# Optimization experiments

Measured on AMD Instinct MI355X. Metric: run time of the kernel, lower is better.

## Reference

```python
import jax, jax.numpy as jnp
import numpy as np

B, H, N, D = 16, 2048, 1024, 2048  # batch, seq len, vocab_size, d_model (= 2*vocab)
KAPPA = 1.0
SCALE = 0.02  # std for materialized params (original inits to zeros -> trivial output)


def setup_inputs() -> dict:
    key = jax.random.key(0)
    kz, kf, kv, kw = jax.random.split(key, 4)
    z = jax.random.randint(kz, (B, H), 0, N)
    F_mat = jax.random.normal(kf, (D, D), jnp.float32) * SCALE
    V = jax.random.normal(kv, (D, D), jnp.float32) * SCALE
    W = jax.random.normal(kw, (D, D), jnp.float32) * SCALE
    return {"z": z, "F_mat": F_mat, "V": V, "W": W}


def reference(z, F_mat, V, W):
    # x[b,t] = e_{z[b,t]} + e_{N + z[b,t-1]},  x[b,0] = e_{z[b,0]}  (E / E_tilde basis rows)
    z_prev = jnp.roll(z, 1, axis=1).at[:, 0].set(0)
    E_z = jax.nn.one_hot(z, D, dtype=jnp.float32)          # [B,H,D]
    x = E_z + jax.nn.one_hot(z_prev + N, D, dtype=jnp.float32)
    x = x.at[:, 0, :].set(E_z[:, 0, :])

    x_H = x[:, -1, :]                                      # [B,D] single query
    W_x = jnp.einsum('bhd,ed->bhe', x, W)                  # x @ W.T -> [B,H,D]
    scores = jnp.einsum('bd,bhd->bh', x_H, W_x)            # [B,H]
    attn = jax.nn.softmax(scores, axis=-1)                 # att_type='softmax'
    weighted_sum = jnp.einsum('bh,bhd->bd', attn, x)       # [B,D]

    # U.T @ (.) just takes the first N coordinates (U = E.T, identity columns)
    xi_A = (weighted_sum @ V.T)[:, :N]                     # [B,N]
    combined = x_H + KAPPA * weighted_sum
    xi_F = (combined @ F_mat.T)[:, :N]                     # [B,N]
    xi = xi_A + xi_F
    # match torch output shape [B, N, 1]
    return xi[..., None], xi_A[..., None], xi_F[..., None]
```

## Files before the change

### kernel.cpp

```cpp
#include <hip/hip_runtime.h>

#define BB 16
#define HH 2048
#define NN 1024
#define DD 2048


__global__ __launch_bounds__(1024) void ot_phase1(const int* __restrict__ z,
                                                  const float* __restrict__ W,
                                                  int* __restrict__ hdr,
                                                  float* __restrict__ wsT) {
    __shared__ int   zsh[HH];
    __shared__ float w1s[DD];
    __shared__ float w2s[DD];
    __shared__ float ws[DD];
    __shared__ float red[16];

    const int b    = blockIdx.x;
    const int tid  = threadIdx.x;
    const int lane = tid & 63;
    const int wid  = tid >> 6;

    ((int2*)zsh)[tid] = ((const int2*)(z + (size_t)b * HH))[tid];
    ws[tid] = 0.f;
    ws[tid + 1024] = 0.f;
    __syncthreads();

    const int d1 = zsh[HH - 1];
    const int d2 = zsh[HH - 2] + NN;

    if (tid < 512) ((float4*)w1s)[tid]       = ((const float4*)(W + (size_t)d1 * DD))[tid];
    else           ((float4*)w2s)[tid - 512] = ((const float4*)(W + (size_t)d2 * DD))[tid - 512];
    __syncthreads();

    const int h0 = tid * 2, h1 = h0 + 1;
    const int z0 = zsh[h0], z1 = zsh[h1];
    const int p0 = (h0 > 0) ? zsh[h0 - 1] + NN : 0;
    const int p1 = z0 + NN;

    float s0 = w1s[z0] + w2s[z0];
    if (h0 > 0) s0 += w1s[p0] + w2s[p0];
    float s1 = w1s[z1] + w2s[z1] + w1s[p1] + w2s[p1];

    float m = fmaxf(s0, s1);
#pragma unroll
    for (int off = 32; off > 0; off >>= 1) m = fmaxf(m, __shfl_xor(m, off));
    if (lane == 0) red[wid] = m;
    __syncthreads();
    float mx = red[0];
#pragma unroll
    for (int i = 1; i < 16; ++i) mx = fmaxf(mx, red[i]);

    const float e0 = __expf(s0 - mx);
    const float e1 = __expf(s1 - mx);
    float t = e0 + e1;
#pragma unroll
    for (int off = 32; off > 0; off >>= 1) t += __shfl_xor(t, off);
    __syncthreads();
    if (lane == 0) red[wid] = t;
    __syncthreads();
    float tot = red[0];
#pragma unroll
    for (int i = 1; i < 16; ++i) tot += red[i];
    const float inv = 1.f / tot;

    atomicAdd(&ws[z0], e0);
    if (h0 > 0) atomicAdd(&ws[p0], e0);
    atomicAdd(&ws[z1], e1);
    atomicAdd(&ws[p1], e1);
    __syncthreads();

    if (tid < 512) {
        float4 o;
        o.x = ws[4 * tid + 0] * inv;
        o.y = ws[4 * tid + 1] * inv;
        o.z = ws[4 * tid + 2] * inv;
        o.w = ws[4 * tid + 3] * inv;
        ((float4*)wsT)[(size_t)tid * BB + b] = o;
    }
    if (tid == 0) { hdr[b] = d1; hdr[BB + b] = d2; }
}

__global__ __launch_bounds__(512) void ot_phase2(const float* __restrict__ V,
                                                 const float* __restrict__ F,
                                                 const int* __restrict__ hdr,
                                                 const float* __restrict__ wsT,
                                                 float* __restrict__ out) {
    const int tid  = threadIdx.x;
    const int lane = tid & 63;
    const int w    = tid >> 6;
    const int bq   = lane & 15;
    const int q    = lane >> 4;
    const int slot = w * 4 + q;
    const int n0   = blockIdx.x;
    const int n1   = n0 + 512;

    const float4* __restrict__ V0 = (const float4*)(V + (size_t)n0 * DD);
    const float4* __restrict__ F0 = (const float4*)(F + (size_t)n0 * DD);
    const float4* __restrict__ V1 = (const float4*)(V + (size_t)n1 * DD);
    const float4* __restrict__ F1 = (const float4*)(F + (size_t)n1 * DD);
    const float4* __restrict__ WS = (const float4*)wsT;

    float a0 = 0.f, f0 = 0.f, a1 = 0.f, f1 = 0.f;

#pragma unroll 4
    for (int it = 0; it < 16; ++it) {
        const int dg = it * 32 + slot;
        float4 s  = WS[(size_t)dg * BB + bq];
        float4 v0 = V0[dg];
        float4 g0 = F0[dg];
        float4 v1 = V1[dg];
        float4 g1 = F1[dg];
        a0 += v0.x * s.x + v0.y * s.y + v0.z * s.z + v0.w * s.w;
        f0 += g0.x * s.x + g0.y * s.y + g0.z * s.z + g0.w * s.w;
        a1 += v1.x * s.x + v1.y * s.y + v1.z * s.z + v1.w * s.w;
        f1 += g1.x * s.x + g1.y * s.y + g1.z * s.z + g1.w * s.w;
    }

#pragma unroll
    for (int off = 16; off <= 32; off <<= 1) {
        a0 += __shfl_xor(a0, off);
        f0 += __shfl_xor(f0, off);
        a1 += __shfl_xor(a1, off);
        f1 += __shfl_xor(f1, off);
    }

    __shared__ float red[4][8][BB];
    if (lane < 16) {
        red[0][w][bq] = a0;
        red[1][w][bq] = f0;
        red[2][w][bq] = a1;
        red[3][w][bq] = f1;
    }
    __syncthreads();

    if (tid < BB) {
        const int b = tid;
        float A0 = 0.f, Fv0 = 0.f, A1 = 0.f, Fv1 = 0.f;
#pragma unroll
        for (int ww = 0; ww < 8; ++ww) {
            A0  += red[0][ww][b];
            Fv0 += red[1][ww][b];
            A1  += red[2][ww][b];
            Fv1 += red[3][ww][b];
        }
        const int e1i = hdr[b], e2i = hdr[BB + b];
        const float* __restrict__ Fr0 = F + (size_t)n0 * DD;
        const float* __restrict__ Fr1 = F + (size_t)n1 * DD;
        Fv0 += Fr0[e1i] + Fr0[e2i];
        Fv1 += Fr1[e1i] + Fr1[e2i];
        out[(size_t)b * NN + n0]            = A0 + Fv0;
        out[(size_t)(BB + b) * NN + n0]     = A0;
        out[(size_t)(2 * BB + b) * NN + n0] = Fv0;
        out[(size_t)b * NN + n1]            = A1 + Fv1;
        out[(size_t)(BB + b) * NN + n1]     = A1;
        out[(size_t)(2 * BB + b) * NN + n1] = Fv1;
    }
}

extern "C" void kernel_launch(void* const* d_in, const int* in_sizes, int n_in,
                              void* d_out, int out_size, void* d_ws, size_t ws_size,
                              hipStream_t stream) {
    const int*   z     = (const int*)d_in[0];
    const float* F_mat = (const float*)d_in[1];
    const float* V     = (const float*)d_in[2];
    const float* W     = (const float*)d_in[3];
    float* out = (float*)d_out;

    int*   hdr = (int*)d_ws;
    float* wsT = (float*)((char*)d_ws + 128);

    ot_phase1<<<BB, 1024, 0, stream>>>(z, W, hdr, wsT);
    ot_phase2<<<NN / 2, 512, 0, stream>>>(V, F_mat, hdr, wsT, out);
}
```

Measured before the change: 25.77 us.

## Pack attention sums to bf16, process four output rows per block, prefetch W row

Phase 1 now reads the last two tokens directly and issues the W row loads before the z tile is staged, which removes one barrier. It also stores the normalized weighted sums as packed bf16. Phase 2 preloads each thread's weighted-sum slice into registers once and processes four V/F rows per block instead of two, so each slice is reused across eight dot products and the wsT traffic is halved. The bf16 packing adds rounding error to the weighted sums, and the larger per-thread register set may limit occupancy.

```diff
diff --git a/kernel.cpp b/kernel.cpp
--- a/kernel.cpp
+++ b/kernel.cpp
@@ -4,36 +4,45 @@
 #define HH 2048
 #define NN 1024
 #define DD 2048
+#define DG (DD / 4)
 
+
+__device__ __forceinline__ unsigned short f2bf(float f) {
+    unsigned u = __float_as_uint(f);
+    u += 0x7fffu + ((u >> 16) & 1u);
+    return (unsigned short)(u >> 16);
+}
 
 __global__ __launch_bounds__(1024) void ot_phase1(const int* __restrict__ z,
                                                   const float* __restrict__ W,
                                                   int* __restrict__ hdr,
-                                                  float* __restrict__ wsT) {
+                                                  uint2* __restrict__ wsB) {
     __shared__ int   zsh[HH];
     __shared__ float w1s[DD];
     __shared__ float w2s[DD];
-    __shared__ float ws[DD];
-    __shared__ float red[16];
+    __shared__ float wsh[DD];
+    __shared__ float redm[16], redt[16];
 
     const int b    = blockIdx.x;
     const int tid  = threadIdx.x;
     const int lane = tid & 63;
     const int wid  = tid >> 6;
 
+    const int4 zt = ((const int4*)(z + (size_t)b * HH))[DG - 1];
+    const int d1 = zt.w;
+    const int d2 = zt.z + NN;
+
+    float4 wv;
+    if (tid < 512) wv = ((const float4*)(W + (size_t)d1 * DD))[tid];
+    else           wv = ((const float4*)(W + (size_t)d2 * DD))[tid - 512];
+
     ((int2*)zsh)[tid] = ((const int2*)(z + (size_t)b * HH))[tid];
-    ws[tid] = 0.f;
-    ws[tid + 1024] = 0.f;
+    wsh[tid] = 0.f; wsh[tid + 1024] = 0.f;
+    if (tid < 512) ((float4*)w1s)[tid] = wv;
+    else           ((float4*)w2s)[tid - 512] = wv;
     __syncthreads();
 
-    const int d1 = zsh[HH - 1];
-    const int d2 = zsh[HH - 2] + NN;
-
-    if (tid < 512) ((float4*)w1s)[tid]       = ((const float4*)(W + (size_t)d1 * DD))[tid];
-    else           ((float4*)w2s)[tid - 512] = ((const float4*)(W + (size_t)d2 * DD))[tid - 512];
-    __syncthreads();
-
-    const int h0 = tid * 2, h1 = h0 + 1;
+    const int h0 = 2 * tid, h1 = h0 + 1;
     const int z0 = zsh[h0], z1 = zsh[h1];
     const int p0 = (h0 > 0) ? zsh[h0 - 1] + NN : 0;
     const int p1 = z0 + NN;
@@ -45,131 +54,134 @@
     float m = fmaxf(s0, s1);
 #pragma unroll
     for (int off = 32; off > 0; off >>= 1) m = fmaxf(m, __shfl_xor(m, off));
-    if (lane == 0) red[wid] = m;
+    if (lane == 0) redm[wid] = m;
     __syncthreads();
-    float mx = red[0];
+    float mx = redm[0];
 #pragma unroll
-    for (int i = 1; i < 16; ++i) mx = fmaxf(mx, red[i]);
+    for (int i = 1; i < 16; ++i) mx = fmaxf(mx, redm[i]);
 
     const float e0 = __expf(s0 - mx);
     const float e1 = __expf(s1 - mx);
     float t = e0 + e1;
 #pragma unroll
     for (int off = 32; off > 0; off >>= 1) t += __shfl_xor(t, off);
+    if (lane == 0) redt[wid] = t;
     __syncthreads();
-    if (lane == 0) red[wid] = t;
-    __syncthreads();
-    float tot = red[0];
+    float tot = 0.f;
 #pragma unroll
-    for (int i = 1; i < 16; ++i) tot += red[i];
+    for (int i = 0; i < 16; ++i) tot += redt[i];
     const float inv = 1.f / tot;
 
-    atomicAdd(&ws[z0], e0);
-    if (h0 > 0) atomicAdd(&ws[p0], e0);
-    atomicAdd(&ws[z1], e1);
-    atomicAdd(&ws[p1], e1);
+    atomicAdd(&wsh[z0], e0);
+    if (h0 > 0) atomicAdd(&wsh[p0], e0);
+    atomicAdd(&wsh[z1], e1);
+    atomicAdd(&wsh[p1], e1);
     __syncthreads();
 
-    if (tid < 512) {
-        float4 o;
-        o.x = ws[4 * tid + 0] * inv;
-        o.y = ws[4 * tid + 1] * inv;
-        o.z = ws[4 * tid + 2] * inv;
-        o.w = ws[4 * tid + 3] * inv;
-        ((float4*)wsT)[(size_t)tid * BB + b] = o;
+    if (tid < DG) {
+        uint2 p;
+        p.x = (unsigned)f2bf(wsh[4 * tid + 0] * inv)
+            | ((unsigned)f2bf(wsh[4 * tid + 1] * inv) << 16);
+        p.y = (unsigned)f2bf(wsh[4 * tid + 2] * inv)
+            | ((unsigned)f2bf(wsh[4 * tid + 3] * inv) << 16);
+        wsB[(size_t)tid * BB + b] = p;
     }
     if (tid == 0) { hdr[b] = d1; hdr[BB + b] = d2; }
 }
 
-__global__ __launch_bounds__(512) void ot_phase2(const float* __restrict__ V,
-                                                 const float* __restrict__ F,
-                                                 const int* __restrict__ hdr,
-                                                 const float* __restrict__ wsT,
-                                                 float* __restrict__ out) {
+__global__ __launch_bounds__(512, 4) void ot_phase2(const float* __restrict__ V,
+                                                    const float* __restrict__ F,
+                                                    const int* __restrict__ hdr,
+                                                    const uint2* __restrict__ wsB,
+                                                    float* __restrict__ out) {
     const int tid  = threadIdx.x;
     const int lane = tid & 63;
     const int w    = tid >> 6;
-    const int bq   = lane & 15;
-    const int q    = lane >> 4;
-    const int slot = w * 4 + q;
-    const int n0   = blockIdx.x;
-    const int n1   = n0 + 512;
+    const int b    = lane & 15;
+    const int s    = tid >> 4;
+    const int g    = blockIdx.x;
 
-    const float4* __restrict__ V0 = (const float4*)(V + (size_t)n0 * DD);
-    const float4* __restrict__ F0 = (const float4*)(F + (size_t)n0 * DD);
-    const float4* __restrict__ V1 = (const float4*)(V + (size_t)n1 * DD);
-    const float4* __restrict__ F1 = (const float4*)(F + (size_t)n1 * DD);
-    const float4* __restrict__ WS = (const float4*)wsT;
+    uint2 wsr[16];
+#pragma unroll
+    for (int i = 0; i < 16; ++i) wsr[i] = wsB[(size_t)(s + 32 * i) * BB + b];
 
-    float a0 = 0.f, f0 = 0.f, a1 = 0.f, f1 = 0.f;
+    const float4* __restrict__ Vr0 = (const float4*)(V + (size_t)(4 * g + 0) * DD);
+    const float4* __restrict__ Vr1 = (const float4*)(V + (size_t)(4 * g + 1) * DD);
+    const float4* __restrict__ Vr2 = (const float4*)(V + (size_t)(4 * g + 2) * DD);
+    const float4* __restrict__ Vr3 = (const float4*)(V + (size_t)(4 * g + 3) * DD);
+    const float4* __restrict__ Fr0 = (const float4*)(F + (size_t)(4 * g + 0) * DD);
+    const float4* __restrict__ Fr1 = (const float4*)(F + (size_t)(4 * g + 1) * DD);
+    const float4* __restrict__ Fr2 = (const float4*)(F + (size_t)(4 * g + 2) * DD);
+    const float4* __restrict__ Fr3 = (const float4*)(F + (size_t)(4 * g + 3) * DD);
 
-#pragma unroll 4
+    float acc[8];
+#pragma unroll
+    for (int j = 0; j < 8; ++j) acc[j] = 0.f;
+
+#pragma unroll
     for (int it = 0; it < 16; ++it) {
-        const int dg = it * 32 + slot;
-        float4 s  = WS[(size_t)dg * BB + bq];
-        float4 v0 = V0[dg];
-        float4 g0 = F0[dg];
-        float4 v1 = V1[dg];
-        float4 g1 = F1[dg];
-        a0 += v0.x * s.x + v0.y * s.y + v0.z * s.z + v0.w * s.w;
-        f0 += g0.x * s.x + g0.y * s.y + g0.z * s.z + g0.w * s.w;
-        a1 += v1.x * s.x + v1.y * s.y + v1.z * s.z + v1.w * s.w;
-        f1 += g1.x * s.x + g1.y * s.y + g1.z * s.z + g1.w * s.w;
+        const int dg = s + 32 * it;
+        const uint2 p = wsr[it];
+        const float s0 = __uint_as_float(p.x << 16);
+        const float s1 = __uint_as_float(p.x & 0xffff0000u);
+        const float s2 = __uint_as_float(p.y << 16);
+        const float s3 = __uint_as_float(p.y & 0xffff0000u);
+        float4 v0 = Vr0[dg], v1 = Vr1[dg], v2 = Vr2[dg], v3 = Vr3[dg];
+        float4 f0 = Fr0[dg], f1 = Fr1[dg], f2 = Fr2[dg], f3 = Fr3[dg];
+        acc[0] += v0.x * s0 + v0.y * s1 + v0.z * s2 + v0.w * s3;
+        acc[1] += f0.x * s0 + f0.y * s1 + f0.z * s2 + f0.w * s3;
+        acc[2] += v1.x * s0 + v1.y * s1 + v1.z * s2 + v1.w * s3;
+        acc[3] += f1.x * s0 + f1.y * s1 + f1.z * s2 + f1.w * s3;
+        acc[4] += v2.x * s0 + v2.y * s1 + v2.z * s2 + v2.w * s3;
+        acc[5] += f2.x * s0 + f2.y * s1 + f2.z * s2 + f2.w * s3;
+        acc[6] += v3.x * s0 + v3.y * s1 + v3.z * s2 + v3.w * s3;
+        acc[7] += f3.x * s0 + f3.y * s1 + f3.z * s2 + f3.w * s3;
     }
 
 #pragma unroll
-    for (int off = 16; off <= 32; off <<= 1) {
-        a0 += __shfl_xor(a0, off);
-        f0 += __shfl_xor(f0, off);
-        a1 += __shfl_xor(a1, off);
-        f1 += __shfl_xor(f1, off);
+    for (int j = 0; j < 8; ++j) {
+        float p = acc[j];
+        p += __shfl_xor(p, 16);
+        p += __shfl_xor(p, 32);
+        acc[j] = p;
     }
 
-    __shared__ float red[4][8][BB];
+    __shared__ float red[8][8][BB];
     if (lane < 16) {
-        red[0][w][bq] = a0;
-        red[1][w][bq] = f0;
-        red[2][w][bq] = a1;
-        red[3][w][bq] = f1;
+#pragma unroll
+        for (int j = 0; j < 8; ++j) red[j][w][b] = acc[j];
     }
     __syncthreads();
 
-    if (tid < BB) {
-        const int b = tid;
-        float A0 = 0.f, Fv0 = 0.f, A1 = 0.f, Fv1 = 0.f;
+    if (tid < 64) {
+        const int r = tid >> 4, bb = tid & 15;
+        float A = 0.f, Fv = 0.f;
 #pragma unroll
         for (int ww = 0; ww < 8; ++ww) {
-            A0  += red[0][ww][b];
-            Fv0 += red[1][ww][b];
-            A1  += red[2][ww][b];
-            Fv1 += red[3][ww][b];
+            A  += red[2 * r + 0][ww][bb];
+            Fv += red[2 * r + 1][ww][bb];
         }
-        const int e1i = hdr[b], e2i = hdr[BB + b];
-        const float* __restrict__ Fr0 = F + (size_t)n0 * DD;
-        const float* __restrict__ Fr1 = F + (size_t)n1 * DD;
-        Fv0 += Fr0[e1i] + Fr0[e2i];
-        Fv1 += Fr1[e1i] + Fr1[e2i];
-        out[(size_t)b * NN + n0]            = A0 + Fv0;
-        out[(size_t)(BB + b) * NN + n0]     = A0;
-        out[(size_t)(2 * BB + b) * NN + n0] = Fv0;
-        out[(size_t)b * NN + n1]            = A1 + Fv1;
-        out[(size_t)(BB + b) * NN + n1]     = A1;
-        out[(size_t)(2 * BB + b) * NN + n1] = Fv1;
+        const int n = 4 * g + r;
+        const float* __restrict__ Fr = F + (size_t)n * DD;
+        Fv += Fr[hdr[bb]] + Fr[hdr[BB + bb]];
+        out[(size_t)bb * NN + n]            = A + Fv;
+        out[(size_t)(BB + bb) * NN + n]     = A;
+        out[(size_t)(2 * BB + bb) * NN + n] = Fv;
     }
 }
 
 extern "C" void kernel_launch(void* const* d_in, const int* in_sizes, int n_in,
                               void* d_out, int out_size, void* d_ws, size_t ws_size,
                               hipStream_t stream) {
-    const int*   z     = (const int*)d_in[0];
-    const float* F_mat = (const float*)d_in[1];
-    const float* V     = (const float*)d_in[2];
-    const float* W     = (const float*)d_in[3];
+    const int*   z  = (const int*)d_in[0];
+    const float* Fm = (const float*)d_in[1];
+    const float* Vm = (const float*)d_in[2];
+    const float* Wm = (const float*)d_in[3];
     float* out = (float*)d_out;
 
     int*   hdr = (int*)d_ws;
-    float* wsT = (float*)((char*)d_ws + 128);
+    uint2* wsB = (uint2*)((char*)d_ws + 128);
 
-    ot_phase1<<<BB, 1024, 0, stream>>>(z, W, hdr, wsT);
-    ot_phase2<<<NN / 2, 512, 0, stream>>>(V, F_mat, hdr, wsT, out);
+    ot_phase1<<<BB, 1024, 0, stream>>>(z, Wm, hdr, wsB);
+    ot_phase2<<<NN / 4, 512, 0, stream>>>(Vm, Fm, hdr, wsB, out);
 }
```

After: 24.35 us. 1.06x faster.
